# Optimization experiments

Hardware: AMD Instinct MI355X
Metric: run time of the kernel (lower is better)

Reference implementation:

```python
import jax, jax.numpy as jnp
import numpy as np

B, C, H, W = 8, 256, 128, 128
K = 3                      # kernel_size
GC = 16                    # group_channels
G = C // GC                # groups = 16
RED = 4                    # reduction_ratio (hardcoded in module)
CR = C // RED              # 64
PAD = (K - 1) // 2


def setup_inputs() -> dict:
    key = jax.random.key(0)
    ks = jax.random.split(key, 8)
    s = 0.05
    return {
        "x":  jax.random.normal(ks[0], (B, C, H, W), dtype=jnp.float32),
        # conv1[0]: 1x1 Conv2d(C, C//4)
        "w1": jax.random.normal(ks[1], (CR, C), dtype=jnp.float32) * s,
        "b1": jax.random.normal(ks[2], (CR,), dtype=jnp.float32) * s,
        # conv1[1]: depthwise KxK Conv2d(C//4, C//4, groups=C//4), padding=K//2
        "wd": jax.random.normal(ks[3], (CR, 1, K, K), dtype=jnp.float32) * s,
        "bd": jax.random.normal(ks[4], (CR,), dtype=jnp.float32) * s,
        # conv2: 1x1 Conv2d(C//4, K*K*G)
        "w2": jax.random.normal(ks[5], (K * K * G, CR), dtype=jnp.float32) * s,
        "b2": jax.random.normal(ks[6], (K * K * G,), dtype=jnp.float32) * s,
    }


def _forward(x, w1, b1, wd, bd, w2, b2):
    # weight generation branch: 1x1 conv -> depthwise KxK conv -> 1x1 conv
    y = jnp.einsum("oc,bchw->bohw", w1, x) + b1[None, :, None, None]
    y = jax.lax.conv_general_dilated(
        y, wd, window_strides=(1, 1),
        padding=[(PAD, PAD), (PAD, PAD)],
        feature_group_count=CR,
        dimension_numbers=("NCHW", "OIHW", "NCHW"),
    ) + bd[None, :, None, None]
    w = jnp.einsum("oc,bchw->bohw", w2, y) + b2[None, :, None, None]
    w = w.reshape(B, G, K, K, H, W)  # per-pixel dynamic depthwise weights

    # involution-style per-pixel depthwise conv, stride=1, padding=(K-1)//2
    xr = x.reshape(B, G, GC, H, W)
    xp = jnp.pad(xr, ((0, 0), (0, 0), (0, 0), (PAD, PAD), (PAD, PAD)))
    out = jnp.zeros((B, G, GC, H, W), dtype=x.dtype)
    for kh in range(K):          # small fixed structural loop (K*K = 9 taps)
        for kw in range(K):
            out = out + xp[:, :, :, kh:kh + H, kw:kw + W] * w[:, :, kh, kw][:, :, None, :, :]
    return out.reshape(B, C, H, W)


def reference(x, w1, b1, wd, bd, w2, b2):
    return _forward(x, w1, b1, wd, bd, w2, b2)
```

## Files before the change

### kernel.cpp

```cpp
#include <hip/hip_runtime.h>
#include <hip/hip_bf16.h>

#define HW    16384
#define IMW   128
#define IMH   128
#define CIN   256
#define CR    64
#define G     16
#define GC    16

typedef __attribute__((ext_vector_type(8))) short short8;
typedef __attribute__((ext_vector_type(4))) float floatx4;

static __device__ __forceinline__ short f2bf(float f) {
  union { float f; unsigned u; } v; v.f = f;
  unsigned r = v.u + 0x7fffu + ((v.u >> 16) & 1u);
  return (short)(r >> 16);
}
static __device__ __forceinline__ float bf2f(short s) {
  union { unsigned u; float f; } v; v.u = ((unsigned)(unsigned short)s) << 16;
  return v.f;
}

__global__ __launch_bounds__(256) void k_cvt_w1(const float* __restrict__ w1,
                                                short* __restrict__ w1b) {
  const int i = blockIdx.x * 256 + threadIdx.x;
  w1b[i] = f2bf(w1[i]);
}

__global__ __launch_bounds__(256) void k_conv1_mfma(const float* __restrict__ x,
                                                    const short* __restrict__ w1b,
                                                    const float* __restrict__ b1,
                                                    short* __restrict__ y1b) {
  const int blk  = blockIdx.x;
  const int b    = blk >> 8;
  const int pt   = blk & 255;
  const int wave = threadIdx.x >> 6;
  const int lane = threadIdx.x & 63;
  const int quad = lane >> 4;
  const int l16  = lane & 15;
  const int p    = pt * 64 + wave * 16 + l16;

  const float* xb = x + (size_t)b * CIN * HW + p;

  floatx4 acc[4];
#pragma unroll
  for (int mt = 0; mt < 4; ++mt)
#pragma unroll
    for (int r = 0; r < 4; ++r) acc[mt][r] = b1[mt * 16 + quad * 4 + r];

#pragma unroll 1
  for (int kk = 0; kk < CIN; kk += 32) {
    short8 afrag[4];
#pragma unroll
    for (int mt = 0; mt < 4; ++mt)
      afrag[mt] = *(const short8*)(w1b + (mt * 16 + l16) * CIN + kk + quad * 8);
    float xv[8];
#pragma unroll
    for (int j = 0; j < 8; ++j)
      xv[j] = xb[(size_t)(kk + quad * 8 + j) * HW];
    short8 bfrag;
#pragma unroll
    for (int j = 0; j < 8; ++j) bfrag[j] = f2bf(xv[j]);
#pragma unroll
    for (int mt = 0; mt < 4; ++mt)
      acc[mt] = __builtin_amdgcn_mfma_f32_16x16x32_bf16(afrag[mt], bfrag, acc[mt], 0, 0, 0);
  }

  short* yb = y1b + (size_t)b * CR * HW + p;
#pragma unroll
  for (int mt = 0; mt < 4; ++mt)
#pragma unroll
    for (int r = 0; r < 4; ++r)
      yb[(size_t)(mt * 16 + quad * 4 + r) * HW] = f2bf(acc[mt][r]);
}

__global__ __launch_bounds__(256) void k_dw(const short* __restrict__ y1b,
                                            const float* __restrict__ wd,
                                            const float* __restrict__ bd,
                                            short* __restrict__ y2b) {
  const int blk   = blockIdx.x;
  const int strip = blk & 15;
  const int c     = (blk >> 4) & 63;
  const int b     = blk >> 10;
  const int w     = threadIdx.x & 127;
  const int rg    = threadIdx.x >> 7;
  const int r0    = strip * 8 + rg * 4;

  const short* src = y1b + (size_t)(b * CR + c) * HW;

  const int   wm1 = w > 0 ? w - 1 : 0;
  const int   wp1 = w < IMW - 1 ? w + 1 : IMW - 1;
  const float mcl = w > 0 ? 1.f : 0.f;
  const float mcr = w < IMW - 1 ? 1.f : 0.f;

  float rowv[6][3];
#pragma unroll
  for (int i = 0; i < 6; ++i) {
    const int rr = r0 - 1 + i;
    const int rc = rr < 0 ? 0 : (rr > IMH - 1 ? IMH - 1 : rr);
    const float mr = (rr < 0 || rr > IMH - 1) ? 0.f : 1.f;
    const short* row = src + rc * IMW;
    rowv[i][0] = mr * mcl * bf2f(row[wm1]);
    rowv[i][1] = mr * bf2f(row[w]);
    rowv[i][2] = mr * mcr * bf2f(row[wp1]);
  }

  float wv[9];
#pragma unroll
  for (int j = 0; j < 9; ++j) wv[j] = wd[c * 9 + j];
  const float bias = bd[c];

  short* dst = y2b + (size_t)(b * CR + c) * HW + r0 * IMW + w;
#pragma unroll
  for (int i = 0; i < 4; ++i) {
    float acc = bias;
#pragma unroll
    for (int kh = 0; kh < 3; ++kh)
#pragma unroll
      for (int kw = 0; kw < 3; ++kw)
        acc += wv[kh * 3 + kw] * rowv[i + kh][kw];
    dst[i * IMW] = f2bf(acc);
  }
}

__global__ __launch_bounds__(256) void k_conv2invol(const float* __restrict__ x,
                                                    const short* __restrict__ y2b,
                                                    const float* __restrict__ w2,
                                                    const float* __restrict__ b2,
                                                    float* __restrict__ out) {
  const int blk  = blockIdx.x;
  const int tile = blk & 63;
  const int gp   = (blk >> 6) & 7;
  const int b    = blk >> 9;
  const int g0   = gp * 2;
  const int tid  = threadIdx.x;
  const int tr   = tid >> 4;
  const int tc   = tid & 15;
  const int h    = (tile >> 3) * 16 + tr;
  const int w    = (tile & 7) * 16 + tc;
  const int p    = h * IMW + w;

  float wv[2][9];
#pragma unroll
  for (int q = 0; q < 2; ++q)
#pragma unroll
    for (int j = 0; j < 9; ++j) wv[q][j] = b2[(g0 + q) * 9 + j];

  const short* y2p = y2b + (size_t)b * CR * HW + p;
#pragma unroll 1
  for (int c = 0; c < CR; c += 4) {
    const float v0 = bf2f(y2p[(size_t)(c + 0) * HW]);
    const float v1 = bf2f(y2p[(size_t)(c + 1) * HW]);
    const float v2 = bf2f(y2p[(size_t)(c + 2) * HW]);
    const float v3 = bf2f(y2p[(size_t)(c + 3) * HW]);
#pragma unroll
    for (int q = 0; q < 2; ++q)
#pragma unroll
      for (int j = 0; j < 9; ++j) {
        const float4 wq = *(const float4*)(w2 + ((g0 + q) * 9 + j) * CR + c);
        wv[q][j] += wq.x * v0 + wq.y * v1 + wq.z * v2 + wq.w * v3;
      }
  }

  const int   hcl[3] = {h > 0 ? h - 1 : 0, h, h < IMH - 1 ? h + 1 : IMH - 1};
  const int   wcl[3] = {w > 0 ? w - 1 : 0, w, w < IMW - 1 ? w + 1 : IMW - 1};
  const float mr[3]  = {h > 0 ? 1.f : 0.f, 1.f, h < IMH - 1 ? 1.f : 0.f};
  const float mc[3]  = {w > 0 ? 1.f : 0.f, 1.f, w < IMW - 1 ? 1.f : 0.f};
  int rel[9];
#pragma unroll
  for (int kh = 0; kh < 3; ++kh)
#pragma unroll
    for (int kw = 0; kw < 3; ++kw) {
      rel[kh * 3 + kw] = hcl[kh] * IMW + wcl[kw];
      const float m = mr[kh] * mc[kw];
      wv[0][kh * 3 + kw] *= m;
      wv[1][kh * 3 + kw] *= m;
    }

  const float* xb = x + (size_t)b * CIN * HW;
  float*       ob = out + (size_t)b * CIN * HW;

#pragma unroll
  for (int q = 0; q < 2; ++q) {
#pragma unroll 2
    for (int cc = 0; cc < GC; ++cc) {
      const int ch = (g0 + q) * GC + cc;
      const float* xp = xb + (size_t)ch * HW;
      float acc = 0.f;
#pragma unroll
      for (int j = 0; j < 9; ++j) acc += wv[q][j] * xp[rel[j]];
      ob[(size_t)ch * HW + p] = acc;
    }
  }
}

extern "C" void kernel_launch(void* const* d_in, const int* in_sizes, int n_in,
                              void* d_out, int out_size, void* d_ws, size_t ws_size,
                              hipStream_t stream) {
  const float* x  = (const float*)d_in[0];
  const float* w1 = (const float*)d_in[1];
  const float* b1 = (const float*)d_in[2];
  const float* wd = (const float*)d_in[3];
  const float* bd = (const float*)d_in[4];
  const float* w2 = (const float*)d_in[5];
  const float* b2 = (const float*)d_in[6];
  float* out = (float*)d_out;

  short* w1b = (short*)d_ws;
  short* y1b = (short*)((char*)d_ws + 65536);
  short* y2b = y1b + (size_t)8 * CR * HW;

  k_cvt_w1<<<dim3(64), dim3(256), 0, stream>>>(w1, w1b);
  k_conv1_mfma<<<dim3(2048), dim3(256), 0, stream>>>(x, w1b, b1, y1b);
  k_dw<<<dim3(8192), dim3(256), 0, stream>>>(y1b, wd, bd, y2b);
  k_conv2invol<<<dim3(4096), dim3(256), 0, stream>>>(x, y2b, w2, b2, out);
}
```

Baseline: 374.3 us.

## Unroll conv1 K-loop, vectorize depthwise conv, retile involution kernel

The conv1 MFMA loop now handles two 32-wide K slices per iteration, so more global loads are in flight before the MFMAs run. The depthwise kernel is rewritten so each thread computes a 2x8 output patch from 16-byte vector loads with register reuse of neighbouring columns, and the grid shrinks from 8192 to 2048 blocks. The fused conv2/involution kernel moves to 8x32 tiles for wider row coalescing, and its unroll factors are raised. These changes add register pressure and fewer blocks for the depthwise stage, which may lower occupancy.

```diff
diff --git a/kernel.cpp b/kernel.cpp
--- a/kernel.cpp
+++ b/kernel.cpp
@@ -50,21 +50,33 @@
     for (int r = 0; r < 4; ++r) acc[mt][r] = b1[mt * 16 + quad * 4 + r];
 
 #pragma unroll 1
-  for (int kk = 0; kk < CIN; kk += 32) {
-    short8 afrag[4];
+  for (int kk = 0; kk < CIN; kk += 64) {
+    short8 af0[4], af1[4];
+#pragma unroll
+    for (int mt = 0; mt < 4; ++mt) {
+      af0[mt] = *(const short8*)(w1b + (mt * 16 + l16) * CIN + kk + quad * 8);
+      af1[mt] = *(const short8*)(w1b + (mt * 16 + l16) * CIN + kk + 32 + quad * 8);
+    }
+    float xv0[8], xv1[8];
+#pragma unroll
+    for (int j = 0; j < 8; ++j)
+      xv0[j] = xb[(size_t)(kk + quad * 8 + j) * HW];
+#pragma unroll
+    for (int j = 0; j < 8; ++j)
+      xv1[j] = xb[(size_t)(kk + 32 + quad * 8 + j) * HW];
+
+    short8 bf0, bf1;
+#pragma unroll
+    for (int j = 0; j < 8; ++j) bf0[j] = f2bf(xv0[j]);
+#pragma unroll
+    for (int j = 0; j < 8; ++j) bf1[j] = f2bf(xv1[j]);
+
 #pragma unroll
     for (int mt = 0; mt < 4; ++mt)
-      afrag[mt] = *(const short8*)(w1b + (mt * 16 + l16) * CIN + kk + quad * 8);
-    float xv[8];
-#pragma unroll
-    for (int j = 0; j < 8; ++j)
-      xv[j] = xb[(size_t)(kk + quad * 8 + j) * HW];
-    short8 bfrag;
-#pragma unroll
-    for (int j = 0; j < 8; ++j) bfrag[j] = f2bf(xv[j]);
+      acc[mt] = __builtin_amdgcn_mfma_f32_16x16x32_bf16(af0[mt], bf0, acc[mt], 0, 0, 0);
 #pragma unroll
     for (int mt = 0; mt < 4; ++mt)
-      acc[mt] = __builtin_amdgcn_mfma_f32_16x16x32_bf16(afrag[mt], bfrag, acc[mt], 0, 0, 0);
+      acc[mt] = __builtin_amdgcn_mfma_f32_16x16x32_bf16(af1[mt], bf1, acc[mt], 0, 0, 0);
   }
 
   short* yb = y1b + (size_t)b * CR * HW + p;
@@ -80,30 +92,33 @@
                                             const float* __restrict__ bd,
                                             short* __restrict__ y2b) {
   const int blk   = blockIdx.x;
-  const int strip = blk & 15;
-  const int c     = (blk >> 4) & 63;
-  const int b     = blk >> 10;
-  const int w     = threadIdx.x & 127;
-  const int rg    = threadIdx.x >> 7;
-  const int r0    = strip * 8 + rg * 4;
+  const int strip = blk & 3;
+  const int c     = (blk >> 2) & 63;
+  const int b     = blk >> 8;
+  const int tcol  = threadIdx.x & 15;
+  const int trow  = threadIdx.x >> 4;
+  const int r0    = strip * 32 + trow * 2;
+  const int c0    = tcol * 8;
 
   const short* src = y1b + (size_t)(b * CR + c) * HW;
 
-  const int   wm1 = w > 0 ? w - 1 : 0;
-  const int   wp1 = w < IMW - 1 ? w + 1 : IMW - 1;
-  const float mcl = w > 0 ? 1.f : 0.f;
-  const float mcr = w < IMW - 1 ? 1.f : 0.f;
-
-  float rowv[6][3];
-#pragma unroll
-  for (int i = 0; i < 6; ++i) {
+  const float mcl = c0 > 0 ? 1.f : 0.f;
+  const float mcr = c0 + 8 < IMW ? 1.f : 0.f;
+  const int   cl  = c0 > 0 ? c0 - 1 : 0;
+  const int   crr = c0 + 8 < IMW ? c0 + 8 : IMW - 1;
+
+  float f[4][10];
+#pragma unroll
+  for (int i = 0; i < 4; ++i) {
     const int rr = r0 - 1 + i;
     const int rc = rr < 0 ? 0 : (rr > IMH - 1 ? IMH - 1 : rr);
     const float mr = (rr < 0 || rr > IMH - 1) ? 0.f : 1.f;
     const short* row = src + rc * IMW;
-    rowv[i][0] = mr * mcl * bf2f(row[wm1]);
-    rowv[i][1] = mr * bf2f(row[w]);
-    rowv[i][2] = mr * mcr * bf2f(row[wp1]);
+    const short8 v = *(const short8*)(row + c0);
+#pragma unroll
+    for (int j = 0; j < 8; ++j) f[i][j + 1] = mr * bf2f(v[j]);
+    f[i][0] = mr * mcl * bf2f(row[cl]);
+    f[i][9] = mr * mcr * bf2f(row[crr]);
   }
 
   float wv[9];
@@ -111,16 +126,21 @@
   for (int j = 0; j < 9; ++j) wv[j] = wd[c * 9 + j];
   const float bias = bd[c];
 
-  short* dst = y2b + (size_t)(b * CR + c) * HW + r0 * IMW + w;
-#pragma unroll
-  for (int i = 0; i < 4; ++i) {
-    float acc = bias;
-#pragma unroll
-    for (int kh = 0; kh < 3; ++kh)
-#pragma unroll
-      for (int kw = 0; kw < 3; ++kw)
-        acc += wv[kh * 3 + kw] * rowv[i + kh][kw];
-    dst[i * IMW] = f2bf(acc);
+  short* dst = y2b + (size_t)(b * CR + c) * HW + r0 * IMW + c0;
+#pragma unroll
+  for (int i = 0; i < 2; ++i) {
+    short8 o;
+#pragma unroll
+    for (int xcol = 0; xcol < 8; ++xcol) {
+      float acc = bias;
+#pragma unroll
+      for (int kh = 0; kh < 3; ++kh)
+#pragma unroll
+        for (int kw = 0; kw < 3; ++kw)
+          acc += wv[kh * 3 + kw] * f[i + kh][xcol + kw];
+      o[xcol] = f2bf(acc);
+    }
+    *(short8*)(dst + i * IMW) = o;
   }
 }
 
@@ -135,10 +155,10 @@
   const int b    = blk >> 9;
   const int g0   = gp * 2;
   const int tid  = threadIdx.x;
-  const int tr   = tid >> 4;
-  const int tc   = tid & 15;
-  const int h    = (tile >> 3) * 16 + tr;
-  const int w    = (tile & 7) * 16 + tc;
+  const int tr   = tid >> 5;
+  const int tc   = tid & 31;
+  const int h    = (tile >> 2) * 8 + tr;
+  const int w    = (tile & 3) * 32 + tc;
   const int p    = h * IMW + w;
 
   float wv[2][9];
@@ -148,7 +168,7 @@
     for (int j = 0; j < 9; ++j) wv[q][j] = b2[(g0 + q) * 9 + j];
 
   const short* y2p = y2b + (size_t)b * CR * HW + p;
-#pragma unroll 1
+#pragma unroll 2
   for (int c = 0; c < CR; c += 4) {
     const float v0 = bf2f(y2p[(size_t)(c + 0) * HW]);
     const float v1 = bf2f(y2p[(size_t)(c + 1) * HW]);
@@ -183,7 +203,7 @@
 
 #pragma unroll
   for (int q = 0; q < 2; ++q) {
-#pragma unroll 2
+#pragma unroll 4
     for (int cc = 0; cc < GC; ++cc) {
       const int ch = (g0 + q) * GC + cc;
       const float* xp = xb + (size_t)ch * HW;
@@ -213,6 +233,6 @@
 
   k_cvt_w1<<<dim3(64), dim3(256), 0, stream>>>(w1, w1b);
   k_conv1_mfma<<<dim3(2048), dim3(256), 0, stream>>>(x, w1b, b1, y1b);
-  k_dw<<<dim3(8192), dim3(256), 0, stream>>>(y1b, wd, bd, y2b);
+  k_dw<<<dim3(2048), dim3(256), 0, stream>>>(y1b, wd, bd, y2b);
   k_conv2invol<<<dim3(4096), dim3(256), 0, stream>>>(x, y2b, w2, b2, out);
 }
```

After: 353.3 us. 1.06x faster.
